# Kernel tuning notes

Measured on AMD Instinct MI355X. Metric: run time of the kernel, lower is better.

## Reference

```python
import jax, jax.numpy as jnp
import numpy as np

N_NODES = 80_000
D_IN = 128
D_HID = 128
D_EMB = 64
N_EDGES = 2_560_000
NUM_PEAKS = 40_000
N_TF = 128
N_GENE = 8_000
MLP_HID = 128
N_OUT = 2


def setup_inputs() -> dict:
    key = jax.random.key(0)
    ks = jax.random.split(key, 8)
    x = jax.random.normal(ks[0], (N_NODES, D_IN), jnp.float32)
    edge_index = jax.random.randint(ks[1], (2, N_EDGES), 0, N_NODES)
    tf_index_list = jax.random.randint(ks[2], (N_TF,), 0, N_NODES - NUM_PEAKS)
    gene_index_list = jax.random.randint(ks[3], (N_GENE,), 0, N_NODES - NUM_PEAKS)
    s = lambda k, shp, fan: jax.random.normal(k, shp, jnp.float32) * np.float32(1.0 / np.sqrt(fan))
    W1 = s(ks[4], (D_IN, D_HID), D_IN)
    b1 = jnp.zeros((D_HID,), jnp.float32)
    W2 = s(ks[5], (D_HID, D_EMB), D_HID)
    b2 = jnp.zeros((D_EMB,), jnp.float32)
    Wm1 = s(ks[6], (2 * D_EMB, MLP_HID), 2 * D_EMB)
    bm1 = jnp.zeros((MLP_HID,), jnp.float32)
    Wm2 = s(ks[7], (MLP_HID, N_OUT), MLP_HID)
    bm2 = jnp.zeros((N_OUT,), jnp.float32)
    return dict(x=x, W1=W1, b1=b1, W2=W2, b2=b2, Wm1=Wm1, bm1=bm1, Wm2=Wm2, bm2=bm2,
                edge_index=edge_index, num=NUM_PEAKS,
                tf_index_list=tf_index_list, gene_index_list=gene_index_list)


def _gcn_agg(h, src, dst, n):
    # mean aggregation of neighbor features: agg[i] = mean_{(j->i) in E} h[j]
    deg = jax.ops.segment_sum(jnp.ones((src.shape[0],), h.dtype), dst, num_segments=n)
    agg = jax.ops.segment_sum(h[src], dst, num_segments=n)
    return agg / jnp.maximum(deg, 1.0)[:, None]


def reference(x, W1, b1, W2, b2, Wm1, bm1, Wm2, bm2,
              edge_index, num, tf_index_list, gene_index_list):
    src, dst = edge_index[0], edge_index[1]
    n = x.shape[0]
    # 2-layer GCN (mean aggregation) -> node embeddings [N, D_EMB]
    h = jax.nn.relu(_gcn_agg(x, src, dst, n) @ W1 + b1)
    emb = _gcn_agg(h, src, dst, n) @ W2 + b2
    # split_tensor(emb, num): pX = emb[:num] (unused), gX = emb[num:]
    gX = emb[num:]
    tf_emb = gX[tf_index_list]      # [T, d]
    g_emb = gX[gene_index_list]     # [G, d]
    T, d = tf_emb.shape
    G = g_emb.shape[0]
    # vectorized equivalent of the nested (tf, gene) concat loop; row order = tf*G + g
    combined = jnp.concatenate([
        jnp.broadcast_to(tf_emb[:, None, :], (T, G, d)),
        jnp.broadcast_to(g_emb[None, :, :], (T, G, d)),
    ], axis=-1).reshape(T * G, 2 * d)
    hid = jax.nn.relu(combined @ Wm1 + bm1)
    out = hid @ Wm2 + bm2
    return jax.nn.softmax(out, axis=-1)
```

## Files before the change

### kernel.cpp

```cpp
#include <hip/hip_runtime.h>
#include <math.h>

#define DIM 128
#define DEMB 64
#define CHUNK 8192

typedef __attribute__((ext_vector_type(8))) short bf16x8;
typedef __attribute__((ext_vector_type(4))) float f32x4;


__device__ __forceinline__ unsigned pack_bf16x2(float a, float b) {
    unsigned ua = __float_as_uint(a);
    unsigned ub = __float_as_uint(b);
    ua = (ua + 0x7fffu + ((ua >> 16) & 1u)) >> 16;
    ub = (ub + 0x7fffu + ((ub >> 16) & 1u)) & 0xffff0000u;
    return ua | ub;
}
__device__ __forceinline__ float lo_bf16(unsigned v) { return __uint_as_float(v << 16); }
__device__ __forceinline__ float hi_bf16(unsigned v) { return __uint_as_float(v & 0xffff0000u); }


__global__ __launch_bounds__(256) void convert_kernel(const float* __restrict__ in,
                                                      unsigned* __restrict__ out, int n2) {
    int i = blockIdx.x * 256 + threadIdx.x;
    int stride = gridDim.x * 256;
    for (; i < n2; i += stride) {
        float2 v = reinterpret_cast<const float2*>(in)[i];
        out[i] = pack_bf16x2(v.x, v.y);
    }
}


__global__ __launch_bounds__(256) void prep_w1t(const float* __restrict__ W1,
                                                unsigned* __restrict__ W1t) {
    int i = blockIdx.x * 256 + threadIdx.x;
    if (i >= 128 * 64) return;
    int n = i >> 6, k2 = i & 63;
    float a = W1[(size_t)(2 * k2) * DIM + n];
    float b = W1[(size_t)(2 * k2 + 1) * DIM + n];
    W1t[i] = pack_bf16x2(a, b);
}


__global__ __launch_bounds__(256) void bucket_count(const int* __restrict__ dst,
                                                    int* __restrict__ bcnt,
                                                    int n_edges, int nbuck) {
    __shared__ int h[384];
    for (int i = threadIdx.x; i < nbuck; i += 256) h[i] = 0;
    __syncthreads();
    int i = blockIdx.x * 256 + threadIdx.x;
    int stride = gridDim.x * 256;
    for (; i < n_edges; i += stride) atomicAdd(&h[dst[i] >> 8], 1);
    __syncthreads();
    for (int i2 = threadIdx.x; i2 < nbuck; i2 += 256)
        if (h[i2]) atomicAdd(&bcnt[i2], h[i2]);
}

__global__ __launch_bounds__(512) void bucket_scan(const int* __restrict__ bcnt,
                                                   int* __restrict__ bstart,
                                                   int* __restrict__ bcursor,
                                                   int nbuck, int n_edges) {
    __shared__ int sm[512];
    int tid = threadIdx.x;
    int v = (tid < nbuck) ? bcnt[tid] : 0;
    sm[tid] = v;
    __syncthreads();
    for (int off = 1; off < 512; off <<= 1) {
        int t = (tid >= off) ? sm[tid - off] : 0;
        __syncthreads();
        if (tid >= off) sm[tid] += t;
        __syncthreads();
    }
    if (tid < nbuck) {
        int e = sm[tid] - v;
        bstart[tid] = e;
        bcursor[tid] = e;
    }
    if (tid == 0) bstart[nbuck] = n_edges;
}

__global__ __launch_bounds__(256) void bucket_scatter(const int* __restrict__ src,
                                                      const int* __restrict__ dst,
                                                      int* __restrict__ bcursor,
                                                      unsigned* __restrict__ binned,
                                                      int n_edges, int nbuck) {
    __shared__ unsigned stage[CHUNK];
    __shared__ unsigned short bkt[CHUNK];
    __shared__ int cnt[384], off[384], gbase[384], cur[384];
    __shared__ int sc[256];
    __shared__ int tot0;
    int tid = threadIdx.x;
    int e0 = blockIdx.x * CHUNK;
    int ne = min(CHUNK, n_edges - e0);
    for (int i = tid; i < nbuck; i += 256) cnt[i] = 0;
    __syncthreads();
    for (int j = tid; j < ne; j += 256) atomicAdd(&cnt[dst[e0 + j] >> 8], 1);
    __syncthreads();
    {
        int v0 = (tid < nbuck) ? cnt[tid] : 0;
        sc[tid] = v0;
        __syncthreads();
        for (int o = 1; o < 256; o <<= 1) {
            int t = (tid >= o) ? sc[tid - o] : 0;
            __syncthreads();
            sc[tid] += t;
            __syncthreads();
        }
        if (tid < nbuck) off[tid] = sc[tid] - v0;
        if (tid == 255) tot0 = sc[255];
        __syncthreads();
        int i1 = 256 + tid;
        int v1 = (i1 < nbuck) ? cnt[i1] : 0;
        sc[tid] = v1;
        __syncthreads();
        for (int o = 1; o < 256; o <<= 1) {
            int t = (tid >= o) ? sc[tid - o] : 0;
            __syncthreads();
            sc[tid] += t;
            __syncthreads();
        }
        if (i1 < nbuck) off[i1] = tot0 + sc[tid] - v1;
        __syncthreads();
    }
    for (int b = tid; b < nbuck; b += 256) {
        cur[b] = off[b];
        gbase[b] = cnt[b] ? atomicAdd(&bcursor[b], cnt[b]) : 0;
    }
    __syncthreads();
    for (int j = tid; j < ne; j += 256) {
        int d = dst[e0 + j];
        int s = src[e0 + j];
        int b = d >> 8;
        int p = atomicAdd(&cur[b], 1);
        stage[p] = ((unsigned)s << 8) | (unsigned)(d & 255);
        bkt[p] = (unsigned short)b;
    }
    __syncthreads();
    for (int j = tid; j < ne; j += 256) {
        int b = bkt[j];
        binned[gbase[b] + (j - off[b])] = stage[j];
    }
}

__global__ __launch_bounds__(256) void bucket_csr(const unsigned* __restrict__ binned,
                                                  const int* __restrict__ bstart,
                                                  int* __restrict__ counts,
                                                  int* __restrict__ rowstart,
                                                  int* __restrict__ ssorted,
                                                  int n_nodes) {
    __shared__ int hist[4096];
    __shared__ int psum[256];
    int b = blockIdx.x;
    int bs = bstart[b], be = bstart[b + 1];
    int node0 = b << 8;
    int tid = threadIdx.x;
    for (int i = tid; i < 4096; i += 256) hist[i] = 0;
    __syncthreads();
    for (int j = bs + tid; j < be; j += 256) {
        unsigned e = binned[j];
        int key = (int)((e & 255u) << 4) | (int)((e >> 8) >> 13);
        atomicAdd(&hist[key], 1);
    }
    __syncthreads();
    int loc[16];
    int s = 0;
#pragma unroll
    for (int k = 0; k < 16; k++) {
        loc[k] = s;
        s += hist[tid * 16 + k];
    }
    psum[tid] = s;
    __syncthreads();
    int v = psum[tid];
    int acc = v;
    for (int o = 1; o < 256; o <<= 1) {
        int t = (tid >= o) ? psum[tid - o] : 0;
        __syncthreads();
        psum[tid] += t;
        __syncthreads();
    }
    int excl = psum[tid] - v;
    (void)acc;
#pragma unroll
    for (int k = 0; k < 16; k++) hist[tid * 16 + k] = excl + loc[k];
    int node = node0 + tid;
    if (node < n_nodes) {
        counts[node] = s;
        rowstart[node] = bs + excl;
    }
    __syncthreads();
    for (int j = bs + tid; j < be; j += 256) {
        unsigned e = binned[j];
        int key = (int)((e & 255u) << 4) | (int)((e >> 8) >> 13);
        int p = atomicAdd(&hist[key], 1);
        ssorted[bs + p] = (int)(e >> 8);
    }
}


__global__ __launch_bounds__(256) void agg_kernel(const unsigned* __restrict__ xh,
                                                  const int* __restrict__ rowstart,
                                                  const int* __restrict__ counts,
                                                  const int* __restrict__ ssorted,
                                                  unsigned* __restrict__ Ah, int n_nodes) {
    int wave = (blockIdx.x * 256 + threadIdx.x) >> 6;
    int lane = threadIdx.x & 63;
    if (wave >= n_nodes) return;
    int base = rowstart[wave];
    int deg = counts[wave];
    const unsigned* xp = xh + lane;
    float ax = 0.f, ay = 0.f;
    int j = 0;
    for (; j + 8 <= deg; j += 8) {
        int s0 = ssorted[base + j];
        int s1 = ssorted[base + j + 1];
        int s2 = ssorted[base + j + 2];
        int s3 = ssorted[base + j + 3];
        int s4 = ssorted[base + j + 4];
        int s5 = ssorted[base + j + 5];
        int s6 = ssorted[base + j + 6];
        int s7 = ssorted[base + j + 7];
        unsigned v0 = xp[(size_t)s0 * 64];
        unsigned v1 = xp[(size_t)s1 * 64];
        unsigned v2 = xp[(size_t)s2 * 64];
        unsigned v3 = xp[(size_t)s3 * 64];
        unsigned v4 = xp[(size_t)s4 * 64];
        unsigned v5 = xp[(size_t)s5 * 64];
        unsigned v6 = xp[(size_t)s6 * 64];
        unsigned v7 = xp[(size_t)s7 * 64];
        ax += ((lo_bf16(v0) + lo_bf16(v1)) + (lo_bf16(v2) + lo_bf16(v3))) +
              ((lo_bf16(v4) + lo_bf16(v5)) + (lo_bf16(v6) + lo_bf16(v7)));
        ay += ((hi_bf16(v0) + hi_bf16(v1)) + (hi_bf16(v2) + hi_bf16(v3))) +
              ((hi_bf16(v4) + hi_bf16(v5)) + (hi_bf16(v6) + hi_bf16(v7)));
    }
    for (; j < deg; j++) {
        int s = ssorted[base + j];
        unsigned v = xp[(size_t)s * 64];
        ax += lo_bf16(v);
        ay += hi_bf16(v);
    }
    float inv = 1.f / fmaxf((float)deg, 1.f);
    Ah[(size_t)wave * 64 + lane] = pack_bf16x2(ax * inv, ay * inv);
}


__global__ __launch_bounds__(256) void gemm1_mfma(const unsigned* __restrict__ Ah,
                                                  const unsigned* __restrict__ W1t,
                                                  const float* __restrict__ b1,
                                                  unsigned* __restrict__ Hh, int n_rows) {
    __shared__ unsigned Wt[128 * 68];
    int tid = threadIdx.x;
#pragma unroll
    for (int i = 0; i < 32; i++) {
        int idx = i * 256 + tid;
        Wt[(idx >> 6) * 68 + (idx & 63)] = W1t[idx];
    }
    __syncthreads();
    int wv = tid >> 6, l = tid & 63;
    int r0w = blockIdx.x * 64 + wv * 16;
    int arow = r0w + (l & 15);
    int arowc = min(arow, n_rows - 1);
    int kgrp = l >> 4;
    const bf16x8* ap = reinterpret_cast<const bf16x8*>(Ah + (size_t)arowc * 64);
    bf16x8 afrag[4];
#pragma unroll
    for (int s = 0; s < 4; s++) afrag[s] = ap[s * 4 + kgrp];

    f32x4 acc[8];
#pragma unroll
    for (int nt = 0; nt < 8; nt++) {
        float bias = b1[nt * 16 + (l & 15)];
        acc[nt] = {bias, bias, bias, bias};
    }
#pragma unroll
    for (int s = 0; s < 4; s++) {
#pragma unroll
        for (int nt = 0; nt < 8; nt++) {
            bf16x8 bfrag = *reinterpret_cast<const bf16x8*>(
                &Wt[(nt * 16 + (l & 15)) * 68 + s * 16 + kgrp * 4]);
            acc[nt] = __builtin_amdgcn_mfma_f32_16x16x32_bf16(afrag[s], bfrag, acc[nt], 0, 0, 0);
        }
    }
    bool even = (l & 1) == 0;
#pragma unroll
    for (int nt = 0; nt < 8; nt++) {
#pragma unroll
        for (int j = 0; j < 4; j++) {
            float v = fmaxf(acc[nt][j], 0.f);
            float vp = __shfl_xor(v, 1);
            int r = r0w + ((l >> 4) << 2) + j;
            if (even && r < n_rows) {
                Hh[(size_t)r * 64 + nt * 8 + ((l & 15) >> 1)] = pack_bf16x2(v, vp);
            }
        }
    }
}


__global__ __launch_bounds__(256) void target_kernel(const unsigned* __restrict__ Hh,
                                                     const float* __restrict__ W2,
                                                     const float* __restrict__ b2,
                                                     const int* __restrict__ rowstart,
                                                     const int* __restrict__ counts,
                                                     const int* __restrict__ ssorted,
                                                     const int* __restrict__ dnum,
                                                     const int* __restrict__ tf_idx,
                                                     const int* __restrict__ gene_idx,
                                                     float* __restrict__ emb, int T, int ntar) {
    __shared__ float W2s[DIM * DEMB];
    __shared__ float aggS[4][DIM];
    int tid = threadIdx.x;
    for (int i = 0; i < 8; i++) {
        int idx = (i * 256 + tid) * 4;
        *reinterpret_cast<float4*>(&W2s[idx]) = *reinterpret_cast<const float4*>(&W2[idx]);
    }
    int wv = tid >> 6, lane = tid & 63;
    int i = blockIdx.x * 4 + wv;
    int num = dnum[0];
    if (i < ntar) {
        int idx = (i < T) ? tf_idx[i] : gene_idx[i - T];
        int node = num + idx;
        int base = rowstart[node];
        int deg = counts[node];
        const unsigned* hp = Hh + lane;
        float ax = 0.f, ay = 0.f;
        int j = 0;
        for (; j + 4 <= deg; j += 4) {
            int s0 = ssorted[base + j];
            int s1 = ssorted[base + j + 1];
            int s2 = ssorted[base + j + 2];
            int s3 = ssorted[base + j + 3];
            unsigned v0 = hp[(size_t)s0 * 64];
            unsigned v1 = hp[(size_t)s1 * 64];
            unsigned v2 = hp[(size_t)s2 * 64];
            unsigned v3 = hp[(size_t)s3 * 64];
            ax += (lo_bf16(v0) + lo_bf16(v1)) + (lo_bf16(v2) + lo_bf16(v3));
            ay += (hi_bf16(v0) + hi_bf16(v1)) + (hi_bf16(v2) + hi_bf16(v3));
        }
        for (; j < deg; j++) {
            int s = ssorted[base + j];
            unsigned v = hp[(size_t)s * 64];
            ax += lo_bf16(v);
            ay += hi_bf16(v);
        }
        float inv = 1.f / fmaxf((float)deg, 1.f);
        float2 st = {ax * inv, ay * inv};
        *reinterpret_cast<float2*>(&aggS[wv][2 * lane]) = st;
    }
    __syncthreads();
    if (i < ntar) {
        float e = b2[lane];
#pragma unroll 4
        for (int k = 0; k < DIM; k++) e += aggS[wv][k] * W2s[k * DEMB + lane];
        emb[(size_t)i * DEMB + lane] = e;
    }
}


__global__ __launch_bounds__(128) void ab_kernel(const float* __restrict__ emb,
                                                 const float* __restrict__ Wm1,
                                                 const float* __restrict__ bm1,
                                                 float* __restrict__ AB, int T, int ntar) {
    int i = blockIdx.x;
    int j = threadIdx.x;
    if (i >= ntar) return;
    const float* e = emb + (size_t)i * DEMB;
    int base = (i < T) ? 0 : DEMB;
    float acc = (i < T) ? bm1[j] : 0.f;
#pragma unroll 4
    for (int k = 0; k < DEMB; k++) acc += e[k] * Wm1[(size_t)(base + k) * DIM + j];
    AB[(size_t)i * DIM + j] = acc;
}


__global__ __launch_bounds__(256) void final_kernel(const float* __restrict__ AB,
                                                    const float* __restrict__ Wm2,
                                                    const float* __restrict__ bm2,
                                                    float* __restrict__ out, int T, int G) {
    __shared__ float tfAs[8 * DIM];
    __shared__ float wd[DIM];
    int tid = threadIdx.x;
    int t0 = blockIdx.y * 8;
    int g0 = blockIdx.x * 256;
    {
        int idx = tid * 4;
        int t = t0 + (idx >> 7);
        float4 v = {0, 0, 0, 0};
        if (t < T) v = *reinterpret_cast<const float4*>(&AB[(size_t)t0 * DIM + idx]);
        *reinterpret_cast<float4*>(&tfAs[idx]) = v;
    }
    if (tid < DIM) wd[tid] = Wm2[tid * 2] - Wm2[tid * 2 + 1];
    __syncthreads();
    int g = g0 + tid;
    int gc = min(g, G - 1);
    const float4* gp = reinterpret_cast<const float4*>(AB + (size_t)(T + gc) * DIM);
    float acc[8];
#pragma unroll
    for (int t = 0; t < 8; t++) acc[t] = 0.f;
    for (int kc = 0; kc < 16; kc++) {
        float4 ga = gp[kc * 2];
        float4 gb = gp[kc * 2 + 1];
        float4 wa = *reinterpret_cast<const float4*>(&wd[kc * 8]);
        float4 wb = *reinterpret_cast<const float4*>(&wd[kc * 8 + 4]);
#pragma unroll
        for (int t = 0; t < 8; t++) {
            const float4 ta = *reinterpret_cast<const float4*>(&tfAs[t * DIM + kc * 8]);
            const float4 tb = *reinterpret_cast<const float4*>(&tfAs[t * DIM + kc * 8 + 4]);
            acc[t] += fmaxf(ta.x + ga.x, 0.f) * wa.x;
            acc[t] += fmaxf(ta.y + ga.y, 0.f) * wa.y;
            acc[t] += fmaxf(ta.z + ga.z, 0.f) * wa.z;
            acc[t] += fmaxf(ta.w + ga.w, 0.f) * wa.w;
            acc[t] += fmaxf(tb.x + gb.x, 0.f) * wb.x;
            acc[t] += fmaxf(tb.y + gb.y, 0.f) * wb.y;
            acc[t] += fmaxf(tb.z + gb.z, 0.f) * wb.z;
            acc[t] += fmaxf(tb.w + gb.w, 0.f) * wb.w;
        }
    }
    if (g < G) {
        float bd = bm2[0] - bm2[1];
#pragma unroll
        for (int t = 0; t < 8; t++) {
            if (t0 + t < T) {
                float d = acc[t] + bd;
                float p0 = 1.f / (1.f + __expf(-d));
                float2 r = {p0, 1.f - p0};
                *reinterpret_cast<float2*>(&out[((size_t)(t0 + t) * G + g) * 2]) = r;
            }
        }
    }
}


extern "C" void kernel_launch(void* const* d_in, const int* in_sizes, int n_in,
                              void* d_out, int out_size, void* d_ws, size_t ws_size,
                              hipStream_t stream) {
    const float* x    = (const float*)d_in[0];
    const float* W1   = (const float*)d_in[1];
    const float* b1   = (const float*)d_in[2];
    const float* W2   = (const float*)d_in[3];
    const float* b2   = (const float*)d_in[4];
    const float* Wm1  = (const float*)d_in[5];
    const float* bm1  = (const float*)d_in[6];
    const float* Wm2  = (const float*)d_in[7];
    const float* bm2  = (const float*)d_in[8];
    const int* ei     = (const int*)d_in[9];
    const int* dnum   = (const int*)d_in[10];
    const int* tfidx  = (const int*)d_in[11];
    const int* geidx  = (const int*)d_in[12];
    float* out = (float*)d_out;

    int n_nodes = in_sizes[0] / DIM;
    int n_edges = in_sizes[9] / 2;
    int T = in_sizes[11];
    int G = in_sizes[12];
    int ntar = T + G;
    int nbuck = (n_nodes + 255) >> 8;
    const int* srcp = ei;
    const int* dstp = ei + n_edges;

    char* w = (char*)d_ws;
    size_t o = 0;
    auto alloc = [&](size_t bytes) {
        void* p = w + o;
        o += (bytes + 255) & ~(size_t)255;
        return p;
    };
    unsigned* xh   = (unsigned*)alloc((size_t)n_nodes * 64 * 4);
    unsigned* Hh   = (unsigned*)alloc((size_t)n_nodes * 64 * 4);
    unsigned* Ah   = (unsigned*)alloc((size_t)n_nodes * 64 * 4);
    int* ssorted   = (int*)alloc((size_t)n_edges * 4);
    int* counts    = (int*)alloc((size_t)n_nodes * 4);
    int* rowstart  = (int*)alloc((size_t)n_nodes * 4);
    unsigned* W1t  = (unsigned*)alloc(128 * 64 * 4);
    int* bcnt      = (int*)alloc(2048);
    int* bstart    = (int*)alloc(2048);
    int* bcursor   = (int*)alloc(2048);
    unsigned* binned = Hh;
    float* emb = (float*)Ah;
    float* AB  = (float*)Ah + (4u * 1024u * 1024u / 4u);

    hipMemsetAsync(bcnt, 0, (size_t)nbuck * 4, stream);

    convert_kernel<<<2048, 256, 0, stream>>>(x, xh, n_nodes * 64);
    prep_w1t<<<32, 256, 0, stream>>>(W1, W1t);
    bucket_count<<<1024, 256, 0, stream>>>(dstp, bcnt, n_edges, nbuck);
    bucket_scan<<<1, 512, 0, stream>>>(bcnt, bstart, bcursor, nbuck, n_edges);
    bucket_scatter<<<(n_edges + CHUNK - 1) / CHUNK, 256, 0, stream>>>(srcp, dstp, bcursor,
                                                                      binned, n_edges, nbuck);
    bucket_csr<<<nbuck, 256, 0, stream>>>(binned, bstart, counts, rowstart, ssorted, n_nodes);

    agg_kernel<<<(n_nodes + 3) / 4, 256, 0, stream>>>(xh, rowstart, counts, ssorted, Ah, n_nodes);
    gemm1_mfma<<<(n_nodes + 63) / 64, 256, 0, stream>>>(Ah, W1t, b1, Hh, n_nodes);
    target_kernel<<<(ntar + 3) / 4, 256, 0, stream>>>(Hh, W2, b2, rowstart, counts, ssorted,
                                                      dnum, tfidx, geidx, emb, T, ntar);
    ab_kernel<<<ntar, 128, 0, stream>>>(emb, Wm1, bm1, AB, T, ntar);
    final_kernel<<<dim3((G + 255) / 256, (T + 7) / 8), 256, 0, stream>>>(AB, Wm2, bm2, out, T, G);
}
```

Before: 354.4 us.

## Simplify edge bucketing, widen conversion loads, and unify gather loops with clamped tails

Several changes at once. The bf16 conversion now reads float4 and writes two packed words per thread. The bucket scatter kernel drops the shared-memory staging and local scan, so each edge is written straight to global memory at an atomically claimed slot. The CSR build drops the 4096-bin sub-sort by source and histograms only by destination node. The aggregation loops in agg_kernel and target_kernel now always issue 8 gathers per iteration, clamping indices and masking the tail. The trade-off is less sorted source order within a row (worse gather locality), less coalesced scatter writes, and some redundant loads on the tail.

Result: no change. 348.1 us (-1.8%).

```diff
diff --git a/kernel.cpp b/kernel.cpp
--- a/kernel.cpp
+++ b/kernel.cpp
@@ -21,12 +21,13 @@
 
 
 __global__ __launch_bounds__(256) void convert_kernel(const float* __restrict__ in,
-                                                      unsigned* __restrict__ out, int n2) {
+                                                      unsigned* __restrict__ out, int n4) {
     int i = blockIdx.x * 256 + threadIdx.x;
     int stride = gridDim.x * 256;
-    for (; i < n2; i += stride) {
-        float2 v = reinterpret_cast<const float2*>(in)[i];
-        out[i] = pack_bf16x2(v.x, v.y);
+    for (; i < n4; i += stride) {
+        float4 v = reinterpret_cast<const float4*>(in)[i];
+        uint2 pk = {pack_bf16x2(v.x, v.y), pack_bf16x2(v.z, v.w)};
+        reinterpret_cast<uint2*>(out)[i] = pk;
     }
 }
 
@@ -84,11 +85,7 @@
                                                       int* __restrict__ bcursor,
                                                       unsigned* __restrict__ binned,
                                                       int n_edges, int nbuck) {
-    __shared__ unsigned stage[CHUNK];
-    __shared__ unsigned short bkt[CHUNK];
-    __shared__ int cnt[384], off[384], gbase[384], cur[384];
-    __shared__ int sc[256];
-    __shared__ int tot0;
+    __shared__ int cnt[384], base[384];
     int tid = threadIdx.x;
     int e0 = blockIdx.x * CHUNK;
     int ne = min(CHUNK, n_edges - e0);
@@ -96,49 +93,18 @@
     __syncthreads();
     for (int j = tid; j < ne; j += 256) atomicAdd(&cnt[dst[e0 + j] >> 8], 1);
     __syncthreads();
-    {
-        int v0 = (tid < nbuck) ? cnt[tid] : 0;
-        sc[tid] = v0;
-        __syncthreads();
-        for (int o = 1; o < 256; o <<= 1) {
-            int t = (tid >= o) ? sc[tid - o] : 0;
-            __syncthreads();
-            sc[tid] += t;
-            __syncthreads();
-        }
-        if (tid < nbuck) off[tid] = sc[tid] - v0;
-        if (tid == 255) tot0 = sc[255];
-        __syncthreads();
-        int i1 = 256 + tid;
-        int v1 = (i1 < nbuck) ? cnt[i1] : 0;
-        sc[tid] = v1;
-        __syncthreads();
-        for (int o = 1; o < 256; o <<= 1) {
-            int t = (tid >= o) ? sc[tid - o] : 0;
-            __syncthreads();
-            sc[tid] += t;
-            __syncthreads();
-        }
-        if (i1 < nbuck) off[i1] = tot0 + sc[tid] - v1;
-        __syncthreads();
-    }
     for (int b = tid; b < nbuck; b += 256) {
-        cur[b] = off[b];
-        gbase[b] = cnt[b] ? atomicAdd(&bcursor[b], cnt[b]) : 0;
+        int c = cnt[b];
+        base[b] = c ? atomicAdd(&bcursor[b], c) : 0;
+        cnt[b] = 0;
     }
     __syncthreads();
     for (int j = tid; j < ne; j += 256) {
         int d = dst[e0 + j];
         int s = src[e0 + j];
         int b = d >> 8;
-        int p = atomicAdd(&cur[b], 1);
-        stage[p] = ((unsigned)s << 8) | (unsigned)(d & 255);
-        bkt[p] = (unsigned short)b;
-    }
-    __syncthreads();
-    for (int j = tid; j < ne; j += 256) {
-        int b = bkt[j];
-        binned[gbase[b] + (j - off[b])] = stage[j];
+        int r = atomicAdd(&cnt[b], 1);
+        binned[base[b] + r] = ((unsigned)s << 8) | (unsigned)(d & 255);
     }
 }
 
@@ -148,51 +114,36 @@
                                                   int* __restrict__ rowstart,
                                                   int* __restrict__ ssorted,
                                                   int n_nodes) {
-    __shared__ int hist[4096];
-    __shared__ int psum[256];
+    __shared__ int sm[256], cur[256];
+    __shared__ int cntv[256];
     int b = blockIdx.x;
     int bs = bstart[b], be = bstart[b + 1];
     int node0 = b << 8;
     int tid = threadIdx.x;
-    for (int i = tid; i < 4096; i += 256) hist[i] = 0;
+    cntv[tid] = 0;
+    __syncthreads();
+    for (int j = bs + tid; j < be; j += 256) atomicAdd(&cntv[binned[j] & 255u], 1);
+    __syncthreads();
+    int v = cntv[tid];
+    sm[tid] = v;
+    __syncthreads();
+    for (int off = 1; off < 256; off <<= 1) {
+        int t = (tid >= off) ? sm[tid - off] : 0;
+        __syncthreads();
+        if (tid >= off) sm[tid] += t;
+        __syncthreads();
+    }
+    int excl = sm[tid] - v;
+    int node = node0 + tid;
+    if (node < n_nodes) {
+        counts[node] = v;
+        rowstart[node] = bs + excl;
+    }
+    cur[tid] = excl;
     __syncthreads();
     for (int j = bs + tid; j < be; j += 256) {
         unsigned e = binned[j];
-        int key = (int)((e & 255u) << 4) | (int)((e >> 8) >> 13);
-        atomicAdd(&hist[key], 1);
-    }
-    __syncthreads();
-    int loc[16];
-    int s = 0;
-#pragma unroll
-    for (int k = 0; k < 16; k++) {
-        loc[k] = s;
-        s += hist[tid * 16 + k];
-    }
-    psum[tid] = s;
-    __syncthreads();
-    int v = psum[tid];
-    int acc = v;
-    for (int o = 1; o < 256; o <<= 1) {
-        int t = (tid >= o) ? psum[tid - o] : 0;
-        __syncthreads();
-        psum[tid] += t;
-        __syncthreads();
-    }
-    int excl = psum[tid] - v;
-    (void)acc;
-#pragma unroll
-    for (int k = 0; k < 16; k++) hist[tid * 16 + k] = excl + loc[k];
-    int node = node0 + tid;
-    if (node < n_nodes) {
-        counts[node] = s;
-        rowstart[node] = bs + excl;
-    }
-    __syncthreads();
-    for (int j = bs + tid; j < be; j += 256) {
-        unsigned e = binned[j];
-        int key = (int)((e & 255u) << 4) | (int)((e >> 8) >> 13);
-        int p = atomicAdd(&hist[key], 1);
+        int p = atomicAdd(&cur[(int)(e & 255u)], 1);
         ssorted[bs + p] = (int)(e >> 8);
     }
 }
@@ -210,34 +161,20 @@
     int deg = counts[wave];
     const unsigned* xp = xh + lane;
     float ax = 0.f, ay = 0.f;
-    int j = 0;
-    for (; j + 8 <= deg; j += 8) {
-        int s0 = ssorted[base + j];
-        int s1 = ssorted[base + j + 1];
-        int s2 = ssorted[base + j + 2];
-        int s3 = ssorted[base + j + 3];
-        int s4 = ssorted[base + j + 4];
-        int s5 = ssorted[base + j + 5];
-        int s6 = ssorted[base + j + 6];
-        int s7 = ssorted[base + j + 7];
-        unsigned v0 = xp[(size_t)s0 * 64];
-        unsigned v1 = xp[(size_t)s1 * 64];
-        unsigned v2 = xp[(size_t)s2 * 64];
-        unsigned v3 = xp[(size_t)s3 * 64];
-        unsigned v4 = xp[(size_t)s4 * 64];
-        unsigned v5 = xp[(size_t)s5 * 64];
-        unsigned v6 = xp[(size_t)s6 * 64];
-        unsigned v7 = xp[(size_t)s7 * 64];
-        ax += ((lo_bf16(v0) + lo_bf16(v1)) + (lo_bf16(v2) + lo_bf16(v3))) +
-              ((lo_bf16(v4) + lo_bf16(v5)) + (lo_bf16(v6) + lo_bf16(v7)));
-        ay += ((hi_bf16(v0) + hi_bf16(v1)) + (hi_bf16(v2) + hi_bf16(v3))) +
-              ((hi_bf16(v4) + hi_bf16(v5)) + (hi_bf16(v6) + hi_bf16(v7)));
-    }
-    for (; j < deg; j++) {
-        int s = ssorted[base + j];
-        unsigned v = xp[(size_t)s * 64];
-        ax += lo_bf16(v);
-        ay += hi_bf16(v);
+    int dm1 = deg - 1;
+    for (int j0 = 0; j0 < deg; j0 += 8) {
+        unsigned vv[8];
+#pragma unroll
+        for (int k = 0; k < 8; k++) {
+            int s = ssorted[base + min(j0 + k, dm1)];
+            vv[k] = xp[(size_t)s * 64];
+        }
+#pragma unroll
+        for (int k = 0; k < 8; k++) {
+            unsigned m = (j0 + k <= dm1) ? vv[k] : 0u;
+            ax += lo_bf16(m);
+            ay += hi_bf16(m);
+        }
     }
     float inv = 1.f / fmaxf((float)deg, 1.f);
     Ah[(size_t)wave * 64 + lane] = pack_bf16x2(ax * inv, ay * inv);
@@ -324,24 +261,20 @@
         int deg = counts[node];
         const unsigned* hp = Hh + lane;
         float ax = 0.f, ay = 0.f;
-        int j = 0;
-        for (; j + 4 <= deg; j += 4) {
-            int s0 = ssorted[base + j];
-            int s1 = ssorted[base + j + 1];
-            int s2 = ssorted[base + j + 2];
-            int s3 = ssorted[base + j + 3];
-            unsigned v0 = hp[(size_t)s0 * 64];
-            unsigned v1 = hp[(size_t)s1 * 64];
-            unsigned v2 = hp[(size_t)s2 * 64];
-            unsigned v3 = hp[(size_t)s3 * 64];
-            ax += (lo_bf16(v0) + lo_bf16(v1)) + (lo_bf16(v2) + lo_bf16(v3));
-            ay += (hi_bf16(v0) + hi_bf16(v1)) + (hi_bf16(v2) + hi_bf16(v3));
-        }
-        for (; j < deg; j++) {
-            int s = ssorted[base + j];
-            unsigned v = hp[(size_t)s * 64];
-            ax += lo_bf16(v);
-            ay += hi_bf16(v);
+        int dm1 = deg - 1;
+        for (int j0 = 0; j0 < deg; j0 += 8) {
+            unsigned vv[8];
+#pragma unroll
+            for (int k = 0; k < 8; k++) {
+                int s = ssorted[base + min(j0 + k, dm1)];
+                vv[k] = hp[(size_t)s * 64];
+            }
+#pragma unroll
+            for (int k = 0; k < 8; k++) {
+                unsigned m = (j0 + k <= dm1) ? vv[k] : 0u;
+                ax += lo_bf16(m);
+                ay += hi_bf16(m);
+            }
         }
         float inv = 1.f / fmaxf((float)deg, 1.f);
         float2 st = {ax * inv, ay * inv};
@@ -481,7 +414,7 @@
 
     hipMemsetAsync(bcnt, 0, (size_t)nbuck * 4, stream);
 
-    convert_kernel<<<2048, 256, 0, stream>>>(x, xh, n_nodes * 64);
+    convert_kernel<<<2048, 256, 0, stream>>>(x, xh, n_nodes * 32);
     prep_w1t<<<32, 256, 0, stream>>>(W1, W1t);
     bucket_count<<<1024, 256, 0, stream>>>(dstp, bcnt, n_edges, nbuck);
     bucket_scan<<<1, 512, 0, stream>>>(bcnt, bstart, bcursor, nbuck, n_edges);
```
